# Performance work log

Measured on AMD Instinct MI355X. Metric: run time of the kernel, lower is better.

The kernel has to match this reference:

```python
import jax, jax.numpy as jnp
import numpy as np

N, E, F_IN = 10000, 160000, 256
H1, C1 = 8, 128          # conv1: heads=8, out 128 per head, concat -> 1024
H2, C2 = 1, 64           # conv2: heads=1, out 64
NEG_SLOPE = 0.2


def setup_inputs() -> dict:
    key = jax.random.key(0)
    ks = jax.random.split(key, 10)
    s_in = 1.0 / np.sqrt(F_IN)
    s_h1 = 1.0 / np.sqrt(H1 * C1)
    return {
        "x": jax.random.normal(ks[0], (N, F_IN), dtype=jnp.float32),
        "edge_index": jax.random.randint(ks[1], (2, E), 0, N, dtype=jnp.int64),
        "W1": jax.random.normal(ks[2], (F_IN, H1 * C1), dtype=jnp.float32) * s_in,
        "att_src1": jax.random.normal(ks[3], (H1, C1), dtype=jnp.float32) * 0.1,
        "att_dst1": jax.random.normal(ks[4], (H1, C1), dtype=jnp.float32) * 0.1,
        "b1": jnp.zeros((H1 * C1,), dtype=jnp.float32),
        "W2": jax.random.normal(ks[5], (H1 * C1, H2 * C2), dtype=jnp.float32) * s_h1,
        "att_src2": jax.random.normal(ks[6], (H2, C2), dtype=jnp.float32) * 0.1,
        "att_dst2": jax.random.normal(ks[7], (H2, C2), dtype=jnp.float32) * 0.1,
        "b2": jnp.zeros((H2 * C2,), dtype=jnp.float32),
    }


def gat_conv(x, src, dst, W, att_src, att_dst, b, n):
    """PyG GATConv (eval mode: dropout off), concat=True, add_self_loops handled by caller."""
    H, C = att_src.shape
    h = (x @ W).reshape(n, H, C)                       # [N,H,C]
    a_s = jnp.einsum('nhc,hc->nh', h, att_src)         # [N,H]
    a_d = jnp.einsum('nhc,hc->nh', h, att_dst)         # [N,H]
    e = jax.nn.leaky_relu(a_s[src] + a_d[dst], NEG_SLOPE)  # [Etot,H]
    # softmax over edges grouped by destination node (numerically stable)
    e_max = jax.ops.segment_max(e, dst, num_segments=n)
    e = jnp.exp(e - e_max[dst])
    denom = jax.ops.segment_sum(e, dst, num_segments=n)
    alpha = e / (denom[dst] + 1e-16)                   # [Etot,H]
    msg = h[src] * alpha[:, :, None]                   # [Etot,H,C]
    out = jax.ops.segment_sum(msg, dst, num_segments=n)  # [N,H,C]
    return out.reshape(n, H * C) + b


def reference(x, edge_index, W1, att_src1, att_dst1, b1, W2, att_src2, att_dst2, b2):
    n = x.shape[0]
    loops = jnp.arange(n, dtype=edge_index.dtype)
    src = jnp.concatenate([edge_index[0], loops])
    dst = jnp.concatenate([edge_index[1], loops])
    h = jax.nn.elu(gat_conv(x, src, dst, W1, att_src1, att_dst1, b1, n))
    return gat_conv(h, src, dst, W2, att_src2, att_dst2, b2, n)
```

## Files before the change

kernel.cpp:

```cpp
#include <hip/hip_runtime.h>
#include <cmath>


typedef _Float16 f16x8 __attribute__((ext_vector_type(8)));
typedef float f32x4 __attribute__((ext_vector_type(4)));
typedef unsigned short u16x8 __attribute__((ext_vector_type(8)));

__device__ __forceinline__ float lrelu(float x) { return x > 0.f ? x : 0.2f * x; }
__device__ __forceinline__ unsigned short f2h(float f) {
  _Float16 h = (_Float16)f;
  return __builtin_bit_cast(unsigned short, h);
}
__device__ __forceinline__ float h2f(unsigned short u) {
  return (float)__builtin_bit_cast(_Float16, u);
}

__device__ __forceinline__ void fma8h(float* acc, uint4 v, float e) {
  f16x8 h = __builtin_bit_cast(f16x8, v);
#pragma unroll
  for (int k = 0; k < 8; ++k) acc[k] = fmaf((float)h[k], e, acc[k]);
}

#define GLOAD_LDS16(gsrc, ldst)                                              \
  __builtin_amdgcn_global_load_lds(                                          \
      (const __attribute__((address_space(1))) unsigned int*)(gsrc),         \
      (__attribute__((address_space(3))) unsigned int*)(ldst), 16, 0, 0)


__global__ __launch_bounds__(256) void prep_fused(
    const int* __restrict__ ei, int* __restrict__ counts, int E,
    const float* __restrict__ x, unsigned short* __restrict__ xpk, int N, int MB1,
    const float* __restrict__ W1, unsigned short* __restrict__ w1pk,
    const float* __restrict__ W2, unsigned short* __restrict__ w2pk) {
  const int countB = (E + 255) / 256;
  const int pxB = MB1 * 8;
  int bid = blockIdx.x;
  int t = threadIdx.x;

  if (bid < countB) {
    int e = bid * 256 + t;
    if (e < E) atomicAdd(&counts[ei[E + e]], 1);
    return;
  }
  bid -= countB;
  if (bid < pxB) {
    int mb = bid >> 3, ks = bid & 7;
    int l = t & 63, f = t >> 6;
    int row = mb * 64 + f * 16 + (l & 15);
    int kc = ks * 32 + (l >> 4) * 8;
    float v[8];
#pragma unroll
    for (int j = 0; j < 8; ++j) v[j] = 0.f;
    if (row < N) {
      const float* xr = x + (size_t)row * 256 + kc;
#pragma unroll
      for (int j = 0; j < 8; ++j) v[j] = xr[j];
    }
    u16x8 hv;
#pragma unroll
    for (int j = 0; j < 8; ++j) hv[j] = f2h(v[j]);
    size_t base = (size_t)(mb * 8 + ks) * 2048;
    *(u16x8*)(xpk + base + (size_t)f * 512 + l * 8) = hv;
    return;
  }
  bid -= pxB;
  if (bid < 64) {
    int hb = bid >> 3, ks = bid & 7;
    int l = t & 63, gq = t >> 6;
    for (int g = gq; g < 8; g += 4) {
      int n = hb * 128 + g * 16 + (l & 15);
      int k0 = ks * 32 + (l >> 4) * 8;
      u16x8 hv;
#pragma unroll
      for (int j = 0; j < 8; ++j) hv[j] = f2h(W1[(size_t)(k0 + j) * 1024 + n]);
      size_t base = (size_t)(hb * 8 + ks) * 4096;
      *(u16x8*)(w1pk + base + (size_t)g * 512 + l * 8) = hv;
    }
    return;
  }
  bid -= 64;
  {
    int ks = bid;
    int l = t & 63, g = t >> 6;
    int n = g * 16 + (l & 15);
    int k0 = ks * 32 + (l >> 4) * 8;
    u16x8 hv;
#pragma unroll
    for (int j = 0; j < 8; ++j) hv[j] = f2h(W2[(size_t)(k0 + j) * 64 + n]);
    size_t base = (size_t)ks * 2048;
    *(u16x8*)(w2pk + base + (size_t)g * 512 + l * 8) = hv;
  }
}


__global__ __launch_bounds__(256) void scan_blk(const int* __restrict__ counts,
                                                int* __restrict__ offsets,
                                                int* __restrict__ bsum, int n) {
  __shared__ int lds[256];
  int b = blockIdx.x, t = threadIdx.x, i = b * 256 + t;
  int v = (i < n) ? counts[i] + 1 : 0;
  lds[t] = v;
  __syncthreads();
  for (int off = 1; off < 256; off <<= 1) {
    int tv = (t >= off) ? lds[t - off] : 0;
    __syncthreads();
    lds[t] += tv;
    __syncthreads();
  }
  if (i < n) offsets[i] = lds[t] - v;
  if (t == 255) bsum[b] = lds[255];
}

__global__ __launch_bounds__(256) void scan_apply(int* __restrict__ offsets,
                                                  int* __restrict__ cursors,
                                                  const int* __restrict__ bsum,
                                                  int nb, int n) {
  __shared__ int pre_s;
  int b = blockIdx.x, t = threadIdx.x;
  if (t == 0) {
    int s = 0;
    for (int i = 0; i < b; ++i) s += bsum[i];
    pre_s = s;
    if (b == nb - 1) {
      int tot = s;
      for (int i = b; i < nb; ++i) tot += bsum[i];
      offsets[n] = tot;
    }
  }
  __syncthreads();
  int i = b * 256 + t;
  if (i < n) {
    int o = offsets[i] + pre_s;
    offsets[i] = o;
    cursors[i] = o;
  }
}

__global__ __launch_bounds__(256) void fill_all(const int* __restrict__ ei,
                                                int* __restrict__ cursors,
                                                const int* __restrict__ offsets,
                                                int* __restrict__ list,
                                                int E, int n) {
  int tid = blockIdx.x * 256 + threadIdx.x;
  if (tid < E) {
    int d = ei[E + tid];
    int pos = atomicAdd(&cursors[d], 1);
    list[pos] = ei[tid];
  } else if (tid < E + n) {
    int i = tid - E;
    list[offsets[i + 1] - 1] = i;
  }
}


__global__ __launch_bounds__(512, 4) void gemm1_att(
    const unsigned short* __restrict__ xpk, const unsigned short* __restrict__ w1pk,
    const float* __restrict__ asrc, const float* __restrict__ adst,
    unsigned short* __restrict__ h1b, float* __restrict__ as1,
    float* __restrict__ ad1) {
  extern __shared__ char sm[];
  const int t = threadIdx.x, wid = t >> 6, lane = t & 63;
  const int wr = wid >> 2, wc = wid & 3;
  const int mb = blockIdx.x, hb = blockIdx.y;
  const int m0 = mb * 128;
  const int l15 = lane & 15, l4 = lane >> 4;

  f32x4 acc[4][2] = {};

  auto stage = [&](int buf, int ks) {
    char* base0 = sm + buf * 16384;
    for (int i = wid; i < 16; i += 8) {
      const unsigned short* src;
      int ldsoff;
      if (i < 8) {
        int r = i >> 2;
        src = xpk + (size_t)((2 * mb + r) * 8 + ks) * 2048 + (i & 3) * 512 + lane * 8;
        ldsoff = i * 1024;
      } else {
        int g = i - 8;
        src = w1pk + (size_t)(hb * 8 + ks) * 4096 + g * 512 + lane * 8;
        ldsoff = 8192 + g * 1024;
      }
      GLOAD_LDS16(src, base0 + ldsoff);
    }
  };

  stage(0, 0);
  __syncthreads();
  int buf = 0;
  for (int step = 0; step < 8; ++step) {
    if (step < 7) stage(buf ^ 1, step + 1);
    const char* b = sm + buf * 16384;
    f16x8 ah[4], bh[2];
#pragma unroll
    for (int mf = 0; mf < 4; ++mf)
      ah[mf] = *(const f16x8*)(b + (wr * 4 + mf) * 1024 + lane * 16);
#pragma unroll
    for (int nf = 0; nf < 2; ++nf)
      bh[nf] = *(const f16x8*)(b + 8192 + (wc * 2 + nf) * 1024 + lane * 16);
#pragma unroll
    for (int mf = 0; mf < 4; ++mf)
#pragma unroll
      for (int nf = 0; nf < 2; ++nf)
        acc[mf][nf] = __builtin_amdgcn_mfma_f32_16x16x32_f16(ah[mf], bh[nf], acc[mf][nf], 0, 0, 0);
    __syncthreads();
    buf ^= 1;
  }

  float* parts_s = (float*)sm;
  float* parts_d = (float*)(sm + 2048);
  unsigned short* ctile = (unsigned short*)(sm + 4096);
  float as_c[2], ad_c[2];
#pragma unroll
  for (int nf = 0; nf < 2; ++nf) {
    int col = hb * 128 + wc * 32 + nf * 16 + l15;
    as_c[nf] = asrc[col];
    ad_c[nf] = adst[col];
  }
#pragma unroll
  for (int mf = 0; mf < 4; ++mf) {
    float ss[4] = {0.f, 0.f, 0.f, 0.f}, dd[4] = {0.f, 0.f, 0.f, 0.f};
#pragma unroll
    for (int nf = 0; nf < 2; ++nf)
#pragma unroll
      for (int r = 0; r < 4; ++r) {
        ss[r] += acc[mf][nf][r] * as_c[nf];
        dd[r] += acc[mf][nf][r] * ad_c[nf];
      }
#pragma unroll
    for (int r = 0; r < 4; ++r)
      for (int m = 1; m < 16; m <<= 1) {
        ss[r] += __shfl_xor(ss[r], m);
        dd[r] += __shfl_xor(dd[r], m);
      }
    if (l15 == 0) {
#pragma unroll
      for (int r = 0; r < 4; ++r) {
        int row = wr * 64 + mf * 16 + l4 * 4 + r;
        parts_s[row * 4 + wc] = ss[r];
        parts_d[row * 4 + wc] = dd[r];
      }
    }
#pragma unroll
    for (int nf = 0; nf < 2; ++nf)
#pragma unroll
      for (int r = 0; r < 4; ++r) {
        int row = wr * 64 + mf * 16 + l4 * 4 + r;
        int col = wc * 32 + nf * 16 + l15;
        ctile[row * 128 + col] = f2h(acc[mf][nf][r]);
      }
  }
  __syncthreads();
  if (t < 128) {
    float s = parts_s[t * 4] + parts_s[t * 4 + 1] + parts_s[t * 4 + 2] + parts_s[t * 4 + 3];
    float d = parts_d[t * 4] + parts_d[t * 4 + 1] + parts_d[t * 4 + 2] + parts_d[t * 4 + 3];
    as1[(size_t)(m0 + t) * 8 + hb] = s;
    ad1[(size_t)(m0 + t) * 8 + hb] = d;
  }
#pragma unroll
  for (int rep = 0; rep < 4; ++rep) {
    int e = rep * 4096 + t * 8;
    int row = e >> 7, col = e & 127;
    u16x8 v = *(const u16x8*)(ctile + e);
    *(u16x8*)(h1b + (size_t)(m0 + row) * 1024 + hb * 128 + col) = v;
  }
}


__global__ __launch_bounds__(256) void agg1_gather(
    const unsigned short* __restrict__ h1b, const float* __restrict__ as1,
    const float* __restrict__ ad1, const int* __restrict__ offsets,
    const int* __restrict__ list, const float* __restrict__ b1,
    unsigned short* __restrict__ o1pk, int n) {
  const int w = threadIdx.x >> 6, lane = threadIdx.x & 63;
  const int quad = lane >> 4, li = lane & 15;

  const int c = blockIdx.x & 7;
  const int q = blockIdx.x >> 3;
  const int node = q * 4 + w;
  if (node >= n) return;
  const int beg = offsets[node], end = offsets[node + 1];
  const float adc = ad1[(size_t)node * 8 + c];
  const char* hrow = (const char*)h1b + (size_t)c * 256 + (size_t)li * 16;

  float acc[8] = {};
  float den = 0.f;
  int j = beg + quad;
  int s1 = 0;
  float a0 = 0.f;
  uint4 v0 = make_uint4(0, 0, 0, 0);
  if (j < end) {
    int s0 = list[j];
    if (j + 4 < end) s1 = list[j + 4];
    a0 = as1[(size_t)s0 * 8 + c];
    v0 = *(const uint4*)(hrow + ((unsigned)s0 << 11));
  }
  for (; j + 4 < end; j += 4) {
    int s2 = (j + 8 < end) ? list[j + 8] : 0;
    float a1 = as1[(size_t)s1 * 8 + c];
    uint4 v1 = *(const uint4*)(hrow + ((unsigned)s1 << 11));
    float e = __expf(lrelu(a0 + adc));
    den += e;
    fma8h(acc, v0, e);
    s1 = s2; a0 = a1; v0 = v1;
  }
  if (j < end) {
    float e = __expf(lrelu(a0 + adc));
    den += e;
    fma8h(acc, v0, e);
  }
#pragma unroll
  for (int k = 0; k < 8; ++k) {
    acc[k] += __shfl_xor(acc[k], 16);
    acc[k] += __shfl_xor(acc[k], 32);
  }
  den += __shfl_xor(den, 16);
  den += __shfl_xor(den, 32);
  {
    const float inv = 1.f / (den + 1e-16f);
    const int k0 = 2 * quad;
    float va = acc[k0]     * inv + b1[c * 128 + li * 8 + k0];
    float vb = acc[k0 + 1] * inv + b1[c * 128 + li * 8 + k0 + 1];
    va = va > 0.f ? va : __expf(va) - 1.f;
    vb = vb > 0.f ? vb : __expf(vb) - 1.f;
    unsigned pk = (unsigned)f2h(va) | ((unsigned)f2h(vb) << 16);
    int mb = node >> 6, f = (node >> 4) & 3, l15n = node & 15;
    int ks = 4 * c + (li >> 2), kc = li & 3;
    size_t g = (size_t)(mb * 32 + ks) * 2048 + (size_t)f * 512 +
               (size_t)(kc * 16 + l15n) * 8 + k0;
    *(unsigned*)(o1pk + g) = pk;
  }
}


__global__ __launch_bounds__(256) void gemm2_splitk(
    const unsigned short* __restrict__ o1pk, const unsigned short* __restrict__ w2pk,
    float* __restrict__ h2p, int Mpad) {
  extern __shared__ char sm[];
  const int t = threadIdx.x, wid = t >> 6, lane = t & 63;
  const int wr = wid >> 1, wc = wid & 1;
  const int mb = blockIdx.x, sk = blockIdx.y;
  const int m0 = mb * 64;
  const int l15 = lane & 15, l4 = lane >> 4;

  f32x4 acc[2][2] = {};

  auto stage = [&](int buf, int ks) {
    char* base0 = sm + buf * 8192;
    const unsigned short* ax = o1pk + (size_t)(mb * 32 + ks) * 2048 + lane * 8;
    const unsigned short* bw = w2pk + (size_t)ks * 2048 + lane * 8;
    GLOAD_LDS16(ax + wid * 512, base0 + wid * 1024);
    GLOAD_LDS16(bw + wid * 512, base0 + 4096 + wid * 1024);
  };

  stage(0, sk * 8);
  __syncthreads();
  int buf = 0;
  for (int step = 0; step < 8; ++step) {
    if (step < 7) stage(buf ^ 1, sk * 8 + step + 1);
    const char* b = sm + buf * 8192;
    f16x8 ah[2], bh[2];
#pragma unroll
    for (int mf = 0; mf < 2; ++mf)
      ah[mf] = *(const f16x8*)(b + (wr * 2 + mf) * 1024 + lane * 16);
#pragma unroll
    for (int nf = 0; nf < 2; ++nf)
      bh[nf] = *(const f16x8*)(b + 4096 + (wc * 2 + nf) * 1024 + lane * 16);
#pragma unroll
    for (int mf = 0; mf < 2; ++mf)
#pragma unroll
      for (int nf = 0; nf < 2; ++nf)
        acc[mf][nf] = __builtin_amdgcn_mfma_f32_16x16x32_f16(ah[mf], bh[nf], acc[mf][nf], 0, 0, 0);
    __syncthreads();
    buf ^= 1;
  }

#pragma unroll
  for (int mf = 0; mf < 2; ++mf)
#pragma unroll
    for (int nf = 0; nf < 2; ++nf)
#pragma unroll
      for (int r = 0; r < 4; ++r) {
        int row = wr * 32 + mf * 16 + l4 * 4 + r;
        int col = wc * 32 + nf * 16 + l15;
        h2p[((size_t)sk * Mpad + m0 + row) * 64 + col] = acc[mf][nf][r];
      }
}


__global__ __launch_bounds__(256) void reduce_att2(
    const float* __restrict__ h2p, const float* __restrict__ asrc,
    const float* __restrict__ adst, float* __restrict__ h2,
    float* __restrict__ as2, float* __restrict__ ad2, int Mpad, int n) {
  int w = threadIdx.x >> 6, lane = threadIdx.x & 63;
  int row = blockIdx.x * 4 + w;
  if (row >= n) return;
  float s = 0.f;
#pragma unroll
  for (int sk = 0; sk < 4; ++sk) s += h2p[((size_t)sk * Mpad + row) * 64 + lane];
  h2[(size_t)row * 64 + lane] = s;
  float ds = s * asrc[lane], dd = s * adst[lane];
  for (int o = 32; o; o >>= 1) { ds += __shfl_xor(ds, o); dd += __shfl_xor(dd, o); }
  if (lane == 0) { as2[row] = ds; ad2[row] = dd; }
}


__global__ __launch_bounds__(256) void agg2_gather(
    const float* __restrict__ h2, const float* __restrict__ as2,
    const float* __restrict__ ad2, const int* __restrict__ offsets,
    const int* __restrict__ list, const float* __restrict__ b2,
    float* __restrict__ out, int n) {
  const int wid = threadIdx.x >> 6, lane = threadIdx.x & 63;
  const int cb = (lane & 15) * 4;
  const int jo = lane >> 4;

  const int node = blockIdx.x * 4 + wid;
  if (node >= n) return;
  const int beg = offsets[node], end = offsets[node + 1];
  const float ad = ad2[node];

  float4 acc = make_float4(0.f, 0.f, 0.f, 0.f);
  float den = 0.f;
  for (int j = beg + jo; j < end; j += 4) {
    int s = list[j];
    float e = __expf(lrelu(as2[s] + ad));
    den += e;
    float4 v = *(const float4*)&h2[(size_t)s * 64 + cb];
    acc.x += e * v.x; acc.y += e * v.y; acc.z += e * v.z; acc.w += e * v.w;
  }
  acc.x += __shfl_xor(acc.x, 16); acc.y += __shfl_xor(acc.y, 16);
  acc.z += __shfl_xor(acc.z, 16); acc.w += __shfl_xor(acc.w, 16);
  den += __shfl_xor(den, 16);
  acc.x += __shfl_xor(acc.x, 32); acc.y += __shfl_xor(acc.y, 32);
  acc.z += __shfl_xor(acc.z, 32); acc.w += __shfl_xor(acc.w, 32);
  den += __shfl_xor(den, 32);
  if (jo == 0) {
    float inv = 1.f / (den + 1e-16f);
    float4 r;
    r.x = acc.x * inv + b2[cb];
    r.y = acc.y * inv + b2[cb + 1];
    r.z = acc.z * inv + b2[cb + 2];
    r.w = acc.w * inv + b2[cb + 3];
    *(float4*)&out[(size_t)node * 64 + cb] = r;
  }
}


extern "C" void kernel_launch(void* const* d_in, const int* in_sizes, int n_in,
                              void* d_out, int out_size, void* d_ws, size_t ws_size,
                              hipStream_t stream) {
  const float* x     = (const float*)d_in[0];
  const int*   ei    = (const int*)d_in[1];
  const float* W1    = (const float*)d_in[2];
  const float* asrc1 = (const float*)d_in[3];
  const float* adst1 = (const float*)d_in[4];
  const float* b1    = (const float*)d_in[5];
  const float* W2    = (const float*)d_in[6];
  const float* asrc2 = (const float*)d_in[7];
  const float* adst2 = (const float*)d_in[8];
  const float* b2    = (const float*)d_in[9];
  float* out = (float*)d_out;

  const int N = in_sizes[0] / 256;
  const int E = in_sizes[1] / 2;
  const int T = E + N;
  const int MBB = (N + 127) / 128;
  const int Mpad = MBB * 128;
  const int MB1 = Mpad / 64;
  const int NB = (N + 255) / 256;
  const int NBLK4 = (N + 3) / 4;
  const int NITEMS1 = NBLK4 * 8;

  char* p = (char*)d_ws;
  auto bump = [&](size_t bytes) {
    char* r = p;
    p += (bytes + 255) & ~(size_t)255;
    return r;
  };
  int* counts  = (int*)bump((size_t)N * 4);
  int* offsets = (int*)bump((size_t)(N + 1) * 4);
  int* cursors = (int*)bump((size_t)N * 4);
  int* bsum    = (int*)bump((size_t)NB * 4);
  int* list    = (int*)bump((size_t)T * 4);
  unsigned short* xpk  = (unsigned short*)bump((size_t)Mpad * 256 * 2);
  unsigned short* w1pk = (unsigned short*)bump((size_t)1024 * 256 * 2);
  unsigned short* h1b  = (unsigned short*)bump((size_t)Mpad * 1024 * 2);
  float* as1           = (float*)bump((size_t)Mpad * 8 * 4);
  float* ad1           = (float*)bump((size_t)Mpad * 8 * 4);
  unsigned short* o1pk = (unsigned short*)bump((size_t)Mpad * 1024 * 2);
  unsigned short* w2pk = (unsigned short*)bump((size_t)64 * 1024 * 2);
  float* as2           = (float*)bump((size_t)Mpad * 4);
  float* ad2           = (float*)bump((size_t)Mpad * 4);
  float* h2p = (float*)h1b;
  float* h2  = (float*)xpk;

  hipMemsetAsync(counts, 0, (size_t)N * 4, stream);
  {
    int gridsz = (E + 255) / 256 + MB1 * 8 + 64 + 32;
    prep_fused<<<gridsz, 256, 0, stream>>>(ei, counts, E, x, xpk, N, MB1,
                                           W1, w1pk, W2, w2pk);
  }
  scan_blk<<<NB, 256, 0, stream>>>(counts, offsets, bsum, N);
  scan_apply<<<NB, 256, 0, stream>>>(offsets, cursors, bsum, NB, N);
  fill_all<<<(E + N + 255) / 256, 256, 0, stream>>>(ei, cursors, offsets, list, E, N);

  gemm1_att<<<dim3(MBB, 8), 512, 36864, stream>>>(xpk, w1pk, asrc1, adst1, h1b, as1, ad1);
  agg1_gather<<<NITEMS1, 256, 0, stream>>>(h1b, as1, ad1, offsets, list, b1, o1pk, N);

  gemm2_splitk<<<dim3(Mpad / 64, 4), 256, 16384, stream>>>(o1pk, w2pk, h2p, Mpad);
  reduce_att2<<<(N + 3) / 4, 256, 0, stream>>>(h2p, asrc2, adst2, h2, as2, ad2, Mpad, N);
  agg2_gather<<<NBLK4, 256, 0, stream>>>(h2, as2, ad2, offsets, list, b2, out, N);
}
```

Before: 130.5 us.

## Precompute edge attention weights and fuse split-K GEMM2 with attention reduction

A new edge_e1 kernel computes the exponentiated attention logit per edge and head into a head-major buffer. agg1_gather then reads these contiguous values instead of doing a random as1 gather and an exp in its inner loop. GEMM2 no longer uses split-K: each block runs all 32 K-steps and computes the as2/ad2 dot products in its epilogue, which removes the reduce_att2 kernel and the partial-sum buffer. The cost is an extra kernel launch, an extra row array written in fill_all, and an 8xT float buffer, plus fewer blocks (less parallelism) in GEMM2.

```diff
diff --git a/kernel.cpp b/kernel.cpp
--- a/kernel.cpp
+++ b/kernel.cpp
@@ -10,9 +10,6 @@
 __device__ __forceinline__ unsigned short f2h(float f) {
   _Float16 h = (_Float16)f;
   return __builtin_bit_cast(unsigned short, h);
-}
-__device__ __forceinline__ float h2f(unsigned short u) {
-  return (float)__builtin_bit_cast(_Float16, u);
 }
 
 __device__ __forceinline__ void fma8h(float* acc, uint4 v, float e) {
@@ -140,15 +137,19 @@
                                                 int* __restrict__ cursors,
                                                 const int* __restrict__ offsets,
                                                 int* __restrict__ list,
+                                                int* __restrict__ row,
                                                 int E, int n) {
   int tid = blockIdx.x * 256 + threadIdx.x;
   if (tid < E) {
     int d = ei[E + tid];
     int pos = atomicAdd(&cursors[d], 1);
     list[pos] = ei[tid];
+    row[pos] = d;
   } else if (tid < E + n) {
     int i = tid - E;
-    list[offsets[i + 1] - 1] = i;
+    int pos = offsets[i + 1] - 1;
+    list[pos] = i;
+    row[pos] = i;
   }
 }
 
@@ -267,11 +268,24 @@
 }
 
 
+__global__ __launch_bounds__(256) void edge_e1(
+    const int* __restrict__ list, const int* __restrict__ row,
+    const float* __restrict__ as1, const float* __restrict__ ad1,
+    float* __restrict__ e1, int T, int Tpad) {
+  int pos = blockIdx.x * 256 + threadIdx.x;
+  int c = blockIdx.y;
+  if (pos >= T) return;
+  int s = list[pos], d = row[pos];
+  e1[(size_t)c * Tpad + pos] =
+      __expf(lrelu(as1[(size_t)s * 8 + c] + ad1[(size_t)d * 8 + c]));
+}
+
+
 __global__ __launch_bounds__(256) void agg1_gather(
-    const unsigned short* __restrict__ h1b, const float* __restrict__ as1,
-    const float* __restrict__ ad1, const int* __restrict__ offsets,
-    const int* __restrict__ list, const float* __restrict__ b1,
-    unsigned short* __restrict__ o1pk, int n) {
+    const unsigned short* __restrict__ h1b, const float* __restrict__ e1,
+    const int* __restrict__ offsets, const int* __restrict__ list,
+    const float* __restrict__ b1, unsigned short* __restrict__ o1pk,
+    int n, int Tpad) {
   const int w = threadIdx.x >> 6, lane = threadIdx.x & 63;
   const int quad = lane >> 4, li = lane & 15;
 
@@ -280,34 +294,32 @@
   const int node = q * 4 + w;
   if (node >= n) return;
   const int beg = offsets[node], end = offsets[node + 1];
-  const float adc = ad1[(size_t)node * 8 + c];
   const char* hrow = (const char*)h1b + (size_t)c * 256 + (size_t)li * 16;
+  const float* e1c = e1 + (size_t)c * Tpad;
 
   float acc[8] = {};
   float den = 0.f;
   int j = beg + quad;
   int s1 = 0;
-  float a0 = 0.f;
+  float e0 = 0.f;
   uint4 v0 = make_uint4(0, 0, 0, 0);
   if (j < end) {
     int s0 = list[j];
     if (j + 4 < end) s1 = list[j + 4];
-    a0 = as1[(size_t)s0 * 8 + c];
+    e0 = e1c[j];
     v0 = *(const uint4*)(hrow + ((unsigned)s0 << 11));
   }
   for (; j + 4 < end; j += 4) {
     int s2 = (j + 8 < end) ? list[j + 8] : 0;
-    float a1 = as1[(size_t)s1 * 8 + c];
+    float e1v = e1c[j + 4];
     uint4 v1 = *(const uint4*)(hrow + ((unsigned)s1 << 11));
-    float e = __expf(lrelu(a0 + adc));
-    den += e;
-    fma8h(acc, v0, e);
-    s1 = s2; a0 = a1; v0 = v1;
+    den += e0;
+    fma8h(acc, v0, e0);
+    s1 = s2; e0 = e1v; v0 = v1;
   }
   if (j < end) {
-    float e = __expf(lrelu(a0 + adc));
-    den += e;
-    fma8h(acc, v0, e);
+    den += e0;
+    fma8h(acc, v0, e0);
   }
 #pragma unroll
   for (int k = 0; k < 8; ++k) {
@@ -333,13 +345,14 @@
 }
 
 
-__global__ __launch_bounds__(256) void gemm2_splitk(
+__global__ __launch_bounds__(256) void gemm2_att(
     const unsigned short* __restrict__ o1pk, const unsigned short* __restrict__ w2pk,
-    float* __restrict__ h2p, int Mpad) {
+    const float* __restrict__ asrc, const float* __restrict__ adst,
+    float* __restrict__ h2, float* __restrict__ as2, float* __restrict__ ad2) {
   extern __shared__ char sm[];
   const int t = threadIdx.x, wid = t >> 6, lane = t & 63;
   const int wr = wid >> 1, wc = wid & 1;
-  const int mb = blockIdx.x, sk = blockIdx.y;
+  const int mb = blockIdx.x;
   const int m0 = mb * 64;
   const int l15 = lane & 15, l4 = lane >> 4;
 
@@ -353,11 +366,11 @@
     GLOAD_LDS16(bw + wid * 512, base0 + 4096 + wid * 1024);
   };
 
-  stage(0, sk * 8);
+  stage(0, 0);
   __syncthreads();
   int buf = 0;
-  for (int step = 0; step < 8; ++step) {
-    if (step < 7) stage(buf ^ 1, sk * 8 + step + 1);
+  for (int step = 0; step < 32; ++step) {
+    if (step < 31) stage(buf ^ 1, step + 1);
     const char* b = sm + buf * 8192;
     f16x8 ah[2], bh[2];
 #pragma unroll
@@ -375,33 +388,53 @@
     buf ^= 1;
   }
 
-#pragma unroll
-  for (int mf = 0; mf < 2; ++mf)
+  float* parts_s = (float*)sm;
+  float* parts_d = (float*)(sm + 512);
+  float as_c[2], ad_c[2];
+#pragma unroll
+  for (int nf = 0; nf < 2; ++nf) {
+    int col = wc * 32 + nf * 16 + l15;
+    as_c[nf] = asrc[col];
+    ad_c[nf] = adst[col];
+  }
+#pragma unroll
+  for (int mf = 0; mf < 2; ++mf) {
+    float ss[4] = {0.f, 0.f, 0.f, 0.f}, dd[4] = {0.f, 0.f, 0.f, 0.f};
+#pragma unroll
+    for (int nf = 0; nf < 2; ++nf)
+#pragma unroll
+      for (int r = 0; r < 4; ++r) {
+        ss[r] += acc[mf][nf][r] * as_c[nf];
+        dd[r] += acc[mf][nf][r] * ad_c[nf];
+      }
+#pragma unroll
+    for (int r = 0; r < 4; ++r)
+      for (int m = 1; m < 16; m <<= 1) {
+        ss[r] += __shfl_xor(ss[r], m);
+        dd[r] += __shfl_xor(dd[r], m);
+      }
+    if (l15 == 0) {
+#pragma unroll
+      for (int r = 0; r < 4; ++r) {
+        int row = wr * 32 + mf * 16 + l4 * 4 + r;
+        parts_s[row * 2 + wc] = ss[r];
+        parts_d[row * 2 + wc] = dd[r];
+      }
+    }
 #pragma unroll
     for (int nf = 0; nf < 2; ++nf)
 #pragma unroll
       for (int r = 0; r < 4; ++r) {
         int row = wr * 32 + mf * 16 + l4 * 4 + r;
         int col = wc * 32 + nf * 16 + l15;
-        h2p[((size_t)sk * Mpad + m0 + row) * 64 + col] = acc[mf][nf][r];
-      }
-}
-
-
-__global__ __launch_bounds__(256) void reduce_att2(
-    const float* __restrict__ h2p, const float* __restrict__ asrc,
-    const float* __restrict__ adst, float* __restrict__ h2,
-    float* __restrict__ as2, float* __restrict__ ad2, int Mpad, int n) {
-  int w = threadIdx.x >> 6, lane = threadIdx.x & 63;
-  int row = blockIdx.x * 4 + w;
-  if (row >= n) return;
-  float s = 0.f;
-#pragma unroll
-  for (int sk = 0; sk < 4; ++sk) s += h2p[((size_t)sk * Mpad + row) * 64 + lane];
-  h2[(size_t)row * 64 + lane] = s;
-  float ds = s * asrc[lane], dd = s * adst[lane];
-  for (int o = 32; o; o >>= 1) { ds += __shfl_xor(ds, o); dd += __shfl_xor(dd, o); }
-  if (lane == 0) { as2[row] = ds; ad2[row] = dd; }
+        h2[(size_t)(m0 + row) * 64 + col] = acc[mf][nf][r];
+      }
+  }
+  __syncthreads();
+  if (t < 64) {
+    as2[m0 + t] = parts_s[t * 2] + parts_s[t * 2 + 1];
+    ad2[m0 + t] = parts_d[t * 2] + parts_d[t * 2 + 1];
+  }
 }
 
 
@@ -464,6 +497,7 @@
   const int N = in_sizes[0] / 256;
   const int E = in_sizes[1] / 2;
   const int T = E + N;
+  const int Tpad = (T + 255) & ~255;
   const int MBB = (N + 127) / 128;
   const int Mpad = MBB * 128;
   const int MB1 = Mpad / 64;
@@ -482,6 +516,8 @@
   int* cursors = (int*)bump((size_t)N * 4);
   int* bsum    = (int*)bump((size_t)NB * 4);
   int* list    = (int*)bump((size_t)T * 4);
+  int* rowb    = (int*)bump((size_t)T * 4);
+  float* e1    = (float*)bump((size_t)8 * Tpad * 4);
   unsigned short* xpk  = (unsigned short*)bump((size_t)Mpad * 256 * 2);
   unsigned short* w1pk = (unsigned short*)bump((size_t)1024 * 256 * 2);
   unsigned short* h1b  = (unsigned short*)bump((size_t)Mpad * 1024 * 2);
@@ -491,8 +527,7 @@
   unsigned short* w2pk = (unsigned short*)bump((size_t)64 * 1024 * 2);
   float* as2           = (float*)bump((size_t)Mpad * 4);
   float* ad2           = (float*)bump((size_t)Mpad * 4);
-  float* h2p = (float*)h1b;
-  float* h2  = (float*)xpk;
+  float* h2 = (float*)h1b;
 
   hipMemsetAsync(counts, 0, (size_t)N * 4, stream);
   {
@@ -502,12 +537,12 @@
   }
   scan_blk<<<NB, 256, 0, stream>>>(counts, offsets, bsum, N);
   scan_apply<<<NB, 256, 0, stream>>>(offsets, cursors, bsum, NB, N);
-  fill_all<<<(E + N + 255) / 256, 256, 0, stream>>>(ei, cursors, offsets, list, E, N);
+  fill_all<<<(E + N + 255) / 256, 256, 0, stream>>>(ei, cursors, offsets, list, rowb, E, N);
 
   gemm1_att<<<dim3(MBB, 8), 512, 36864, stream>>>(xpk, w1pk, asrc1, adst1, h1b, as1, ad1);
-  agg1_gather<<<NITEMS1, 256, 0, stream>>>(h1b, as1, ad1, offsets, list, b1, o1pk, N);
-
-  gemm2_splitk<<<dim3(Mpad / 64, 4), 256, 16384, stream>>>(o1pk, w2pk, h2p, Mpad);
-  reduce_att2<<<(N + 3) / 4, 256, 0, stream>>>(h2p, asrc2, adst2, h2, as2, ad2, Mpad, N);
+  edge_e1<<<dim3((T + 255) / 256, 8), 256, 0, stream>>>(list, rowb, as1, ad1, e1, T, Tpad);
+  agg1_gather<<<NITEMS1, 256, 0, stream>>>(h1b, e1, offsets, list, b1, o1pk, N, Tpad);
+
+  gemm2_att<<<Mpad / 64, 256, 16384, stream>>>(o1pk, w2pk, asrc2, adst2, h2, as2, ad2);
   agg2_gather<<<NBLK4, 256, 0, stream>>>(h2, as2, ad2, offsets, list, b2, out, N);
 }
```

Result: slower. 141.2 us (+8.2%).
